# Optimization experiments

Hardware: AMD Instinct MI355X
Metric: run time of the kernel (lower is better)

Reference implementation:

```python
import jax, jax.numpy as jnp
import numpy as np

B, T, D = 2048, 200, 64
H1, H2 = 80, 40
CONST_MIN = -4294967295.0


def setup_inputs() -> dict:
    key = jax.random.key(0)
    ks = jax.random.split(key, 10)
    q = jax.random.normal(ks[0], (B, D), dtype=jnp.float32)
    k = jax.random.normal(ks[1], (B, T, D), dtype=jnp.float32)
    v = jax.random.normal(ks[2], (B, T, D), dtype=jnp.float32)
    mask = jax.random.randint(ks[3], (B, T), 0, 2, dtype=jnp.int32)
    # MLP params: Dense(80, sigmoid) -> Dense(40, sigmoid) -> Dense(1)
    s1 = 1.0 / np.sqrt(4 * D)
    W1 = jax.random.normal(ks[4], (4 * D, H1), dtype=jnp.float32) * s1
    b1 = jnp.zeros((H1,), dtype=jnp.float32)
    W2 = jax.random.normal(ks[5], (H1, H2), dtype=jnp.float32) * (1.0 / np.sqrt(H1))
    b2 = jnp.zeros((H2,), dtype=jnp.float32)
    Wf = jax.random.normal(ks[6], (H2, 1), dtype=jnp.float32) * (1.0 / np.sqrt(H2))
    bf = jnp.zeros((1,), dtype=jnp.float32)
    return {"q": q, "k": k, "v": v, "mask": mask,
            "W1": W1, "b1": b1, "W2": W2, "b2": b2, "Wf": Wf, "bf": bf}


def reference(q, k, v, mask, W1, b1, W2, b2, Wf, bf):
    # q: [B,D] tiled over T -> [B,T,D]
    qt = jnp.broadcast_to(q[:, None, :], k.shape)
    # per-pair features [B,T,4D]
    info = jnp.concatenate([qt, k, qt - k, qt * k], axis=-1)
    h = jax.nn.sigmoid(jnp.einsum('btf,fh->bth', info, W1) + b1)
    h = jax.nn.sigmoid(jnp.einsum('bth,hg->btg', h, W2) + b2)
    logits = (jnp.einsum('btg,go->bto', h, Wf) + bf)[..., 0]  # [B,T]
    logits = jnp.where(mask == 0, jnp.float32(CONST_MIN), logits)
    w = jax.nn.softmax(logits, axis=-1)  # [B,T]
    out = jnp.einsum('bt,btd->bd', w, v)  # weighted sum of v
    return out
```

## Files before the change

### kernel.cpp

```cpp
#include <hip/hip_runtime.h>
#include <math.h>

#define T_LEN 200
#define SEG 100
#define NB 2048

typedef short bf8 __attribute__((ext_vector_type(8)));
typedef float f32x4 __attribute__((ext_vector_type(4)));

__device__ __forceinline__ float sigmoidf_(float x){ return 1.0f/(1.0f+__expf(-x)); }
__device__ __forceinline__ unsigned int pk_bf16(float lo, float hi){
  unsigned int r; asm("v_cvt_pk_bf16_f32 %0, %1, %2":"=v"(r):"v"(lo),"v"(hi)); return r;
}
union U4B8 { uint4 u; bf8 b; };
__device__ __forceinline__ bf8 pack8(float4 x, float4 y){
  U4B8 r;
  r.u.x = pk_bf16(x.x,x.y); r.u.y = pk_bf16(x.z,x.w);
  r.u.z = pk_bf16(y.x,y.y); r.u.w = pk_bf16(y.z,y.w);
  return r.b;
}
__device__ __forceinline__ bf8 pack8m(float4 x, float4 qx, float4 y, float4 qy){
  U4B8 r;
  r.u.x = pk_bf16(x.x*qx.x, x.y*qx.y); r.u.y = pk_bf16(x.z*qx.z, x.w*qx.w);
  r.u.z = pk_bf16(y.x*qy.x, y.y*qy.y); r.u.w = pk_bf16(y.z*qy.z, y.w*qy.w);
  return r.b;
}

__global__ void prep_kernel(const float* __restrict__ W1, const float* __restrict__ W2,
                            const float* __restrict__ b2, const float* __restrict__ Wf,
                            float* __restrict__ wsf){
  unsigned short* fb = (unsigned short*)wsf;
  int i = blockIdx.x*256 + threadIdx.x;
  if (i < 15360){
    int fi = i >> 9;
    int lane = (i>>3)&63, e = i&7;
    int ht = fi/6, ks = fi%6;
    int h = ht*16 + (lane&15);
    int f = ks*32 + ((lane>>4)<<3) + e;
    float val;
    if (f < 64)        val = W1[(64+f)*80+h] - W1[(128+f)*80+h];
    else if (f < 128)  val = W1[(128+f)*80+h];
    else               val = W1[(f-128)*80+h] + W1[f*80+h];
    fb[i] = (unsigned short)(pk_bf16(val,val) & 0xffffu);
  }
  if (i < 4608){
    int fi = i >> 9;
    int lane = (i>>3)&63, e = i&7;
    int gt = fi/3, ks = fi%3;
    int g = gt*16 + (lane&15);
    int h = ks*32 + ((lane>>4)<<3) + e;
    float val = (g<40 && h<80) ? W2[h*40+g] : 0.f;
    fb[15360+i] = (unsigned short)(pk_bf16(val,val) & 0xffffu);
  }
  if (i < 48){
    wsf[9984  + i] = (i<40) ? b2[i] : 0.f;
    wsf[10032 + i] = (i<40) ? Wf[i] : 0.f;
  }
}

__global__ __launch_bounds__(64, 1) void fused_partial(
    const float* __restrict__ q, const float* __restrict__ k, const float* __restrict__ v,
    const int* __restrict__ mask, const float* __restrict__ b1,
    const float* __restrict__ bf, const float* __restrict__ wsf,
    float* __restrict__ pvp, float* __restrict__ sep)
{
  __shared__ unsigned short tl[112];
  __shared__ __align__(16) unsigned int Hw[2][16*52];
  __shared__ float e_lds[16];
  __shared__ __align__(16) unsigned int w2s[9*64*4];

  const int lane = threadIdx.x;
  const int lg = lane>>4, lc = lane&15;
  const int bid = blockIdx.x;
  const long b = bid >> 1;
  const int tbase = (bid & 1) * SEG;

  const float* kb = k + b*(T_LEN*64);
  const float* vb = v + b*(T_LEN*64);
  const int*   mb = mask + b*T_LEN;
  const float* qb = q + b*64;
  const unsigned short* fbg = (const unsigned short*)wsf;
  const bf8* A1f = (const bf8*)fbg;
  const uint4* A2u = (const uint4*)(fbg + 15360);
  const float* b2p = wsf + 9984;
  const float* wfp = wsf + 10032;

  { uint4 z = {0,0,0,0}; *(uint4*)(&Hw[lane>>5][((lane&31)>>1)*52 + 40 + (lane&1)*4]) = z; }

  #pragma unroll
  for (int i=0;i<9;++i) ((uint4*)w2s)[i*64+lane] = A2u[i*64+lane];

  bf8 wk[20];
  #pragma unroll
  for (int ht=0; ht<5; ++ht)
    #pragma unroll
    for (int j=0; j<4; ++j) wk[ht*4+j] = A1f[(ht*6+j)*64+lane];
  float b2v[12], wfv[12];
  #pragma unroll
  for (int gt=0; gt<3; ++gt){
    float4 bv = *(const float4*)(b2p + gt*16 + lg*4);
    float4 wv = *(const float4*)(wfp + gt*16 + lg*4);
    b2v[gt*4+0]=bv.x; b2v[gt*4+1]=bv.y; b2v[gt*4+2]=bv.z; b2v[gt*4+3]=bv.w;
    wfv[gt*4+0]=wv.x; wfv[gt*4+1]=wv.y; wfv[gt*4+2]=wv.z; wfv[gt*4+3]=wv.w;
  }

  f32x4 qacc[5];
  float4 qA0 = *(const float4*)(qb + lg*8);
  float4 qA1 = *(const float4*)(qb + lg*8 + 4);
  float4 qB0 = *(const float4*)(qb + 32 + lg*8);
  float4 qB1 = *(const float4*)(qb + 32 + lg*8 + 4);
  {
    bf8 fq0 = pack8(qA0,qA1);
    bf8 fq1 = pack8(qB0,qB1);
    #pragma unroll
    for (int ht=0; ht<5; ++ht){
      float4 bv = *(const float4*)(b1 + ht*16 + lg*4);
      qacc[ht][0]=bv.x; qacc[ht][1]=bv.y; qacc[ht][2]=bv.z; qacc[ht][3]=bv.w;
      qacc[ht] = __builtin_amdgcn_mfma_f32_16x16x32_bf16(A1f[(ht*6+4)*64+lane], fq0, qacc[ht],0,0,0);
      qacc[ht] = __builtin_amdgcn_mfma_f32_16x16x32_bf16(A1f[(ht*6+5)*64+lane], fq1, qacc[ht],0,0,0);
    }
  }
  const float bf0 = bf[0];

  unsigned long long ltm = (1ull<<lane) - 1ull;
  bool f0m = (mb[tbase + lane] != 0);
  unsigned long long bal0 = __ballot(f0m);
  bool f1m = (lane < SEG-64) && (mb[tbase + 64 + lane] != 0);
  unsigned long long bal1 = __ballot(f1m);
  int c0n = (int)__popcll(bal0);
  int tot = c0n + (int)__popcll(bal1);
  if (f0m) tl[(int)__popcll(bal0 & ltm)] = (unsigned short)(tbase + lane);
  if (f1m) tl[c0n + (int)__popcll(bal1 & ltm)] = (unsigned short)(tbase + 64 + lane);
  asm volatile("s_waitcnt lgkmcnt(0)" ::: "memory");
  __builtin_amdgcn_sched_barrier(0);

  if (tot == 0){
    pvp[(long)bid*64 + lane] = 0.f;
    if (lane == 0) sep[bid] = 0.f;
    return;
  }

  int tp = tl[min(lc, tot-1)];
  const float* kr = kb + tp*64 + lg*8;
  float4 na0 = *(const float4*)(kr);
  float4 na1 = *(const float4*)(kr+4);
  float4 nb0 = *(const float4*)(kr+32);
  float4 nb1 = *(const float4*)(kr+36);
  float vcur[16];
  #pragma unroll
  for (int i=0;i<16;++i){
    int ti = tl[min(i, tot-1)];
    vcur[i] = vb[ti*64 + lane];
  }

  float acc_pv0 = 0.f, acc_pv1 = 0.f;
  float se0 = 0.f, se1 = 0.f;
  int buf = 0;
  for (int base = 0; base < tot; base += 16, buf ^= 1){
    const bool have_next = (base + 16 < tot);
    bf8 f0 = pack8(na0,na1);
    bf8 f1 = pack8(nb0,nb1);
    bf8 f2 = pack8m(na0,qA0,na1,qA1);
    bf8 f3 = pack8m(nb0,qB0,nb1,qB1);
    float vnxt[16];
    if (have_next){
      int tn = tl[min(base+16+lc, tot-1)];
      const float* krn = kb + tn*64 + lg*8;
      na0 = *(const float4*)(krn);
      na1 = *(const float4*)(krn+4);
      nb0 = *(const float4*)(krn+32);
      nb1 = *(const float4*)(krn+36);
      #pragma unroll
      for (int i=0;i<16;++i){
        int ti = tl[min(base+16+i, tot-1)];
        vnxt[i] = vb[ti*64 + lane];
      }
    }

    f32x4 acc[5];
    #pragma unroll
    for (int ht=0; ht<5; ++ht) acc[ht] = qacc[ht];
    #pragma unroll
    for (int ht=0; ht<5; ++ht){
      acc[ht] = __builtin_amdgcn_mfma_f32_16x16x32_bf16(wk[ht*4+0], f0, acc[ht],0,0,0);
      acc[ht] = __builtin_amdgcn_mfma_f32_16x16x32_bf16(wk[ht*4+1], f1, acc[ht],0,0,0);
      acc[ht] = __builtin_amdgcn_mfma_f32_16x16x32_bf16(wk[ht*4+2], f2, acc[ht],0,0,0);
      acc[ht] = __builtin_amdgcn_mfma_f32_16x16x32_bf16(wk[ht*4+3], f3, acc[ht],0,0,0);
    }

    unsigned int* Hb = &Hw[buf][0];
    #pragma unroll
    for (int ht=0; ht<5; ++ht){
      #pragma unroll
      for (int rp=0; rp<2; ++rp)
        Hb[lc*52 + ht*8+lg*2+rp] = pk_bf16(sigmoidf_(acc[ht][2*rp]), sigmoidf_(acc[ht][2*rp+1]));
    }
    asm volatile("s_waitcnt lgkmcnt(0)" ::: "memory");
    __builtin_amdgcn_sched_barrier(0);

    bf8 c0[3];
    #pragma unroll
    for (int ks=0; ks<3; ++ks) c0[ks] = *(const bf8*)(Hb + lc*52 + 16*ks + 4*lg);
    f32x4 g0[3];
    #pragma unroll
    for (int gt=0; gt<3; ++gt){
      g0[gt][0]=b2v[gt*4+0]; g0[gt][1]=b2v[gt*4+1]; g0[gt][2]=b2v[gt*4+2]; g0[gt][3]=b2v[gt*4+3];
    }
    #pragma unroll
    for (int gt=0; gt<3; ++gt){
      #pragma unroll
      for (int ks=0; ks<3; ++ks){
        bf8 wf2 = *(const bf8*)(w2s + ((gt*3+ks)*64+lane)*4);
        g0[gt] = __builtin_amdgcn_mfma_f32_16x16x32_bf16(wf2, c0[ks], g0[gt],0,0,0);
      }
    }
    float p0=0.f;
    #pragma unroll
    for (int gt=0; gt<3; ++gt){
      #pragma unroll
      for (int r=0;r<4;++r) p0 = fmaf(wfv[gt*4+r], sigmoidf_(g0[gt][r]), p0);
    }
    p0 += __shfl_xor(p0,16); p0 += __shfl_xor(p0,32);
    if (lg == 0) e_lds[lc] = (base+lc < tot) ? __expf(p0 + bf0) : 0.f;
    asm volatile("s_waitcnt lgkmcnt(0)" ::: "memory");
    __builtin_amdgcn_sched_barrier(0);

    #pragma unroll
    for (int i=0;i<16;i+=2){
      float ei0 = e_lds[i];
      float ei1 = e_lds[i+1];
      se0 += ei0; se1 += ei1;
      acc_pv0 = fmaf(ei0, vcur[i],   acc_pv0);
      acc_pv1 = fmaf(ei1, vcur[i+1], acc_pv1);
    }
    if (have_next){
      #pragma unroll
      for (int i=0;i<16;++i) vcur[i] = vnxt[i];
    }
  }

  pvp[(long)bid*64 + lane] = acc_pv0 + acc_pv1;
  if (lane == 0) sep[bid] = se0 + se1;
}

__global__ __launch_bounds__(64) void combine_kernel(
    const float* __restrict__ v, const float* __restrict__ pvp,
    const float* __restrict__ sep, float* __restrict__ out)
{
  const int lane = threadIdx.x;
  const long b = blockIdx.x;
  float se = sep[2*b] + sep[2*b+1];
  float pv = pvp[(2*b)*64 + lane] + pvp[(2*b+1)*64 + lane];
  if (se > 0.f){
    out[b*64 + lane] = pv / se;
  } else {
    const float* vb = v + b*(T_LEN*64);
    float accv = 0.f;
    for (int t=0; t<T_LEN; ++t) accv += vb[t*64 + lane];
    out[b*64 + lane] = accv * (1.0f/(float)T_LEN);
  }
}

extern "C" void kernel_launch(void* const* d_in, const int* in_sizes, int n_in,
                              void* d_out, int out_size, void* d_ws, size_t ws_size,
                              hipStream_t stream) {
  const float* q    = (const float*)d_in[0];
  const float* k    = (const float*)d_in[1];
  const float* v    = (const float*)d_in[2];
  const int*   mask = (const int*)d_in[3];
  const float* W1   = (const float*)d_in[4];
  const float* b1   = (const float*)d_in[5];
  const float* W2   = (const float*)d_in[6];
  const float* b2   = (const float*)d_in[7];
  const float* Wf   = (const float*)d_in[8];
  const float* bf   = (const float*)d_in[9];
  float* out = (float*)d_out;
  float* wsf = (float*)d_ws;
  float* pvp = wsf + 10240;
  float* sep = wsf + 10240 + 4096*64;

  hipLaunchKernelGGL(prep_kernel, dim3(60), dim3(256), 0, stream, W1, W2, b2, Wf, wsf);
  hipLaunchKernelGGL(fused_partial, dim3(NB*2), dim3(64), 0, stream,
                     q, k, v, mask, b1, bf, wsf, pvp, sep);
  hipLaunchKernelGGL(combine_kernel, dim3(NB), dim3(64), 0, stream,
                     v, pvp, sep, out);
}
```

Before: 44.12 us.

## Fold q-dependent W1 terms into per-batch weights and bias b2 via MFMA

Because each block handles a single batch row, the k and q*k feature blocks of W1 are merged into one q-scaled weight per block (W_k' = Wbc + q*Wd). This halves the first-layer MFMAs per tile from 20 to 10 and removes the per-tile q*k packing. The b2 bias moves into the W2 matrix through a constant-one column in the hidden LDS tile, and the double-buffered H tile, the explicit waitcnt barriers and the V-prefetch pipeline are dropped. The combined weights are rounded to bf16 after the q-multiply, which changes numerics slightly. V is now loaded inside each iteration instead of being prefetched, so its latency may be exposed.

```diff
diff --git a/kernel.cpp b/kernel.cpp
--- a/kernel.cpp
+++ b/kernel.cpp
@@ -11,6 +11,9 @@
 __device__ __forceinline__ float sigmoidf_(float x){ return 1.0f/(1.0f+__expf(-x)); }
 __device__ __forceinline__ unsigned int pk_bf16(float lo, float hi){
   unsigned int r; asm("v_cvt_pk_bf16_f32 %0, %1, %2":"=v"(r):"v"(lo),"v"(hi)); return r;
+}
+__device__ __forceinline__ float bfu(short s){
+  union{unsigned u; float f;} c; c.u = ((unsigned)(unsigned short)s)<<16; return c.f;
 }
 union U4B8 { uint4 u; bf8 b; };
 __device__ __forceinline__ bf8 pack8(float4 x, float4 y){
@@ -19,10 +22,12 @@
   r.u.z = pk_bf16(y.x,y.y); r.u.w = pk_bf16(y.z,y.w);
   return r.b;
 }
-__device__ __forceinline__ bf8 pack8m(float4 x, float4 qx, float4 y, float4 qy){
+__device__ __forceinline__ bf8 combine8(bf8 fbc, bf8 fd, float4 ql, float4 qh){
   U4B8 r;
-  r.u.x = pk_bf16(x.x*qx.x, x.y*qx.y); r.u.y = pk_bf16(x.z*qx.z, x.w*qx.w);
-  r.u.z = pk_bf16(y.x*qy.x, y.y*qy.y); r.u.w = pk_bf16(y.z*qy.z, y.w*qy.w);
+  r.u.x = pk_bf16(fmaf(ql.x, bfu(fd[0]), bfu(fbc[0])), fmaf(ql.y, bfu(fd[1]), bfu(fbc[1])));
+  r.u.y = pk_bf16(fmaf(ql.z, bfu(fd[2]), bfu(fbc[2])), fmaf(ql.w, bfu(fd[3]), bfu(fbc[3])));
+  r.u.z = pk_bf16(fmaf(qh.x, bfu(fd[4]), bfu(fbc[4])), fmaf(qh.y, bfu(fd[5]), bfu(fbc[5])));
+  r.u.w = pk_bf16(fmaf(qh.z, bfu(fd[6]), bfu(fbc[6])), fmaf(qh.w, bfu(fd[7]), bfu(fbc[7])));
   return r.b;
 }
 
@@ -49,11 +54,13 @@
     int gt = fi/3, ks = fi%3;
     int g = gt*16 + (lane&15);
     int h = ks*32 + ((lane>>4)<<3) + e;
-    float val = (g<40 && h<80) ? W2[h*40+g] : 0.f;
+    float val;
+    if (g < 40 && h < 80)       val = W2[h*40+g];
+    else if (g < 40 && h == 80) val = b2[g];
+    else                        val = 0.f;
     fb[15360+i] = (unsigned short)(pk_bf16(val,val) & 0xffffu);
   }
   if (i < 48){
-    wsf[9984  + i] = (i<40) ? b2[i] : 0.f;
     wsf[10032 + i] = (i<40) ? Wf[i] : 0.f;
   }
 }
@@ -65,7 +72,7 @@
     float* __restrict__ pvp, float* __restrict__ sep)
 {
   __shared__ unsigned short tl[112];
-  __shared__ __align__(16) unsigned int Hw[2][16*52];
+  __shared__ __align__(16) unsigned int Hw[16*52];
   __shared__ float e_lds[16];
   __shared__ __align__(16) unsigned int w2s[9*64*4];
 
@@ -82,33 +89,36 @@
   const unsigned short* fbg = (const unsigned short*)wsf;
   const bf8* A1f = (const bf8*)fbg;
   const uint4* A2u = (const uint4*)(fbg + 15360);
-  const float* b2p = wsf + 9984;
   const float* wfp = wsf + 10032;
 
-  { uint4 z = {0,0,0,0}; *(uint4*)(&Hw[lane>>5][((lane&31)>>1)*52 + 40 + (lane&1)*4]) = z; }
+  if (lane < 32){
+    uint4 z = {0,0,0,0};
+    if (!(lane&1)) z.x = 0x00003F80u;
+    *(uint4*)(&Hw[(lane>>1)*52 + 40 + (lane&1)*4]) = z;
+  }
 
   #pragma unroll
   for (int i=0;i<9;++i) ((uint4*)w2s)[i*64+lane] = A2u[i*64+lane];
 
-  bf8 wk[20];
-  #pragma unroll
-  for (int ht=0; ht<5; ++ht)
-    #pragma unroll
-    for (int j=0; j<4; ++j) wk[ht*4+j] = A1f[(ht*6+j)*64+lane];
-  float b2v[12], wfv[12];
-  #pragma unroll
-  for (int gt=0; gt<3; ++gt){
-    float4 bv = *(const float4*)(b2p + gt*16 + lg*4);
-    float4 wv = *(const float4*)(wfp + gt*16 + lg*4);
-    b2v[gt*4+0]=bv.x; b2v[gt*4+1]=bv.y; b2v[gt*4+2]=bv.z; b2v[gt*4+3]=bv.w;
-    wfv[gt*4+0]=wv.x; wfv[gt*4+1]=wv.y; wfv[gt*4+2]=wv.z; wfv[gt*4+3]=wv.w;
-  }
-
-  f32x4 qacc[5];
   float4 qA0 = *(const float4*)(qb + lg*8);
   float4 qA1 = *(const float4*)(qb + lg*8 + 4);
   float4 qB0 = *(const float4*)(qb + 32 + lg*8);
   float4 qB1 = *(const float4*)(qb + 32 + lg*8 + 4);
+
+  bf8 wk[10];
+  #pragma unroll
+  for (int ht=0; ht<5; ++ht){
+    wk[ht*2+0] = combine8(A1f[(ht*6+0)*64+lane], A1f[(ht*6+2)*64+lane], qA0, qA1);
+    wk[ht*2+1] = combine8(A1f[(ht*6+1)*64+lane], A1f[(ht*6+3)*64+lane], qB0, qB1);
+  }
+  float wfv[12];
+  #pragma unroll
+  for (int gt=0; gt<3; ++gt){
+    float4 wv = *(const float4*)(wfp + gt*16 + lg*4);
+    wfv[gt*4+0]=wv.x; wfv[gt*4+1]=wv.y; wfv[gt*4+2]=wv.z; wfv[gt*4+3]=wv.w;
+  }
+
+  f32x4 qacc[5];
   {
     bf8 fq0 = pack8(qA0,qA1);
     bf8 fq1 = pack8(qB0,qB1);
@@ -131,8 +141,6 @@
   int tot = c0n + (int)__popcll(bal1);
   if (f0m) tl[(int)__popcll(bal0 & ltm)] = (unsigned short)(tbase + lane);
   if (f1m) tl[c0n + (int)__popcll(bal1 & ltm)] = (unsigned short)(tbase + 64 + lane);
-  asm volatile("s_waitcnt lgkmcnt(0)" ::: "memory");
-  __builtin_amdgcn_sched_barrier(0);
 
   if (tot == 0){
     pvp[(long)bid*64 + lane] = 0.f;
@@ -146,23 +154,19 @@
   float4 na1 = *(const float4*)(kr+4);
   float4 nb0 = *(const float4*)(kr+32);
   float4 nb1 = *(const float4*)(kr+36);
-  float vcur[16];
-  #pragma unroll
-  for (int i=0;i<16;++i){
-    int ti = tl[min(i, tot-1)];
-    vcur[i] = vb[ti*64 + lane];
-  }
 
   float acc_pv0 = 0.f, acc_pv1 = 0.f;
   float se0 = 0.f, se1 = 0.f;
-  int buf = 0;
-  for (int base = 0; base < tot; base += 16, buf ^= 1){
+  for (int base = 0; base < tot; base += 16){
     const bool have_next = (base + 16 < tot);
     bf8 f0 = pack8(na0,na1);
     bf8 f1 = pack8(nb0,nb1);
-    bf8 f2 = pack8m(na0,qA0,na1,qA1);
-    bf8 f3 = pack8m(nb0,qB0,nb1,qB1);
-    float vnxt[16];
+    float vcur[16];
+    #pragma unroll
+    for (int i=0;i<16;++i){
+      int ti = tl[min(base+i, tot-1)];
+      vcur[i] = vb[ti*64 + lane];
+    }
     if (have_next){
       int tn = tl[min(base+16+lc, tot-1)];
       const float* krn = kb + tn*64 + lg*8;
@@ -170,11 +174,6 @@
       na1 = *(const float4*)(krn+4);
       nb0 = *(const float4*)(krn+32);
       nb1 = *(const float4*)(krn+36);
-      #pragma unroll
-      for (int i=0;i<16;++i){
-        int ti = tl[min(base+16+i, tot-1)];
-        vnxt[i] = vb[ti*64 + lane];
-      }
     }
 
     f32x4 acc[5];
@@ -182,30 +181,23 @@
     for (int ht=0; ht<5; ++ht) acc[ht] = qacc[ht];
     #pragma unroll
     for (int ht=0; ht<5; ++ht){
-      acc[ht] = __builtin_amdgcn_mfma_f32_16x16x32_bf16(wk[ht*4+0], f0, acc[ht],0,0,0);
-      acc[ht] = __builtin_amdgcn_mfma_f32_16x16x32_bf16(wk[ht*4+1], f1, acc[ht],0,0,0);
-      acc[ht] = __builtin_amdgcn_mfma_f32_16x16x32_bf16(wk[ht*4+2], f2, acc[ht],0,0,0);
-      acc[ht] = __builtin_amdgcn_mfma_f32_16x16x32_bf16(wk[ht*4+3], f3, acc[ht],0,0,0);
-    }
-
-    unsigned int* Hb = &Hw[buf][0];
+      acc[ht] = __builtin_amdgcn_mfma_f32_16x16x32_bf16(wk[ht*2+0], f0, acc[ht],0,0,0);
+      acc[ht] = __builtin_amdgcn_mfma_f32_16x16x32_bf16(wk[ht*2+1], f1, acc[ht],0,0,0);
+    }
+
     #pragma unroll
     for (int ht=0; ht<5; ++ht){
       #pragma unroll
       for (int rp=0; rp<2; ++rp)
-        Hb[lc*52 + ht*8+lg*2+rp] = pk_bf16(sigmoidf_(acc[ht][2*rp]), sigmoidf_(acc[ht][2*rp+1]));
-    }
-    asm volatile("s_waitcnt lgkmcnt(0)" ::: "memory");
-    __builtin_amdgcn_sched_barrier(0);
+        Hw[lc*52 + ht*8+lg*2+rp] = pk_bf16(sigmoidf_(acc[ht][2*rp]), sigmoidf_(acc[ht][2*rp+1]));
+    }
 
     bf8 c0[3];
     #pragma unroll
-    for (int ks=0; ks<3; ++ks) c0[ks] = *(const bf8*)(Hb + lc*52 + 16*ks + 4*lg);
+    for (int ks=0; ks<3; ++ks) c0[ks] = *(const bf8*)(Hw + lc*52 + 16*ks + 4*lg);
     f32x4 g0[3];
     #pragma unroll
-    for (int gt=0; gt<3; ++gt){
-      g0[gt][0]=b2v[gt*4+0]; g0[gt][1]=b2v[gt*4+1]; g0[gt][2]=b2v[gt*4+2]; g0[gt][3]=b2v[gt*4+3];
-    }
+    for (int gt=0; gt<3; ++gt){ g0[gt][0]=0.f; g0[gt][1]=0.f; g0[gt][2]=0.f; g0[gt][3]=0.f; }
     #pragma unroll
     for (int gt=0; gt<3; ++gt){
       #pragma unroll
@@ -222,8 +214,6 @@
     }
     p0 += __shfl_xor(p0,16); p0 += __shfl_xor(p0,32);
     if (lg == 0) e_lds[lc] = (base+lc < tot) ? __expf(p0 + bf0) : 0.f;
-    asm volatile("s_waitcnt lgkmcnt(0)" ::: "memory");
-    __builtin_amdgcn_sched_barrier(0);
 
     #pragma unroll
     for (int i=0;i<16;i+=2){
@@ -232,10 +222,6 @@
       se0 += ei0; se1 += ei1;
       acc_pv0 = fmaf(ei0, vcur[i],   acc_pv0);
       acc_pv1 = fmaf(ei1, vcur[i+1], acc_pv1);
-    }
-    if (have_next){
-      #pragma unroll
-      for (int i=0;i<16;++i) vcur[i] = vnxt[i];
     }
   }
 
```

Measured after the change: 43.65 us. About the same (-1.1%).
